# Kernel optimization log

Hardware: AMD Instinct MI355X
Metric: run time of the kernel (lower is better)

Reference implementation:

```python
import jax, jax.numpy as jnp
import numpy as np

# dims
B, S, V, H, D, I, L, SL, P = 1, 2048, 32000, 1024, 512, 4096, 2, 32, 4096
DECAY_FAST, DECAY_SLOW, CONS_RATE, CONS_EVERY = 0.9, 0.99, 0.1, 10


def _ln(x, g, b):
    m = x.mean(-1, keepdims=True)
    v = ((x - m) ** 2).mean(-1, keepdims=True)
    return (x - m) * jax.lax.rsqrt(v + 1e-5) * g + b


def _memory_scan(items, gates, fast0, slow0):
    # items [B,S,D], gates [B,S,SL]; sequential per-timestep memory update
    cons = (jnp.arange(items.shape[1]) % CONS_EVERY) == 0
    def step(carry, x):
        fast, slow = carry
        item, gate, c = x
        fast = DECAY_FAST * fast + gate[:, :, None] * item[:, None, :]
        slow = jnp.where(c, DECAY_SLOW * slow + CONS_RATE * fast, slow)
        fast = jnp.where(c, (1.0 - CONS_RATE) * fast, fast)
        return (fast, slow), None
    (fast, slow), _ = jax.lax.scan(
        step, (fast0, slow0),
        (items.transpose(1, 0, 2), gates.transpose(1, 0, 2), cons))
    return fast, slow


def _forward(input_ids, fast_states, slow_states, emb, pos_emb, W_item, b_item,
             W_q, b_q, rh_W1, rh_b1, rh_W2, rh_b2, gate_W, gate_b, W_out, b_out,
             ln1_g, ln1_b, ffn_W1, ffn_b1, ffn_W2, ffn_b2, ln2_g, ln2_b, fln_g, fln_b):
    b, s = input_ids.shape
    h = emb[input_ids] + pos_emb[:s][None]  # [B,S,H]
    new_fast, new_slow = [], []
    for l in range(W_item.shape[0]):
        items = h @ W_item[l] + b_item[l]          # [B,S,D]
        query = h @ W_q[l] + b_q[l]                # [B,S,H]
        # retrieval head -> unit-norm unbinding keys
        k1 = jax.nn.gelu(items @ rh_W1[l] + rh_b1[l])
        keys = k1 @ rh_W2[l] + rh_b2[l]
        keys = keys / (jnp.linalg.norm(keys, axis=-1, keepdims=True) + 1e-6)
        fast0, slow0 = fast_states[l], slow_states[l]  # [B,SL,D]
        # retrieval uses the initial (constant-within-sequence) states, so it
        # vectorizes over seq: slot attention + hadamard unbinding
        mem = jnp.concatenate([fast0, slow0], axis=1)  # [B,2*SL,D]
        scores = jnp.einsum('bsd,bnd->bsn', keys, mem) / jnp.sqrt(jnp.float32(D))
        attn = jax.nn.softmax(scores, axis=-1)
        retrieved = jnp.einsum('bsn,bnd->bsd', attn, mem) * keys  # [B,S,D]
        gates = jax.nn.sigmoid(jnp.concatenate([h, retrieved], -1) @ gate_W[l] + gate_b[l])
        fast_gates = gates[..., :SL]
        fast, slow = _memory_scan(items, fast_gates, fast0, slow0)
        new_fast.append(fast)
        new_slow.append(slow)
        out = jnp.concatenate([query, retrieved], -1) @ W_out[l] + b_out[l]
        h = _ln(h + out, ln1_g[l], ln1_b[l])
        ffn = jax.nn.gelu(h @ ffn_W1[l] + ffn_b1[l]) @ ffn_W2[l] + ffn_b2[l]
        h = _ln(h + ffn, ln2_g[l], ln2_b[l])
    h = _ln(h, fln_g, fln_b)
    logits = jnp.einsum('bsh,vh->bsv', h, emb)  # tied lm_head
    return logits, jnp.stack(new_fast), jnp.stack(new_slow)


def setup_inputs() -> dict:
    key = jax.random.key(0)
    def rn(i, shape, scale=0.02):
        return jax.random.normal(jax.random.fold_in(key, i), shape, dtype=jnp.float32) * scale
    z = lambda shape: jnp.zeros(shape, jnp.float32)
    return dict(
        input_ids=jax.random.randint(jax.random.fold_in(key, 0), (B, S), 0, V),
        fast_states=rn(100, (L, B, SL, D), 0.5),
        slow_states=rn(101, (L, B, SL, D), 0.5),
        emb=rn(1, (V, H)),
        pos_emb=rn(2, (P, H)),
        W_item=rn(3, (L, H, D)), b_item=z((L, D)),
        W_q=rn(4, (L, H, H)), b_q=z((L, H)),
        rh_W1=rn(5, (L, D, 2 * D)), rh_b1=z((L, 2 * D)),
        rh_W2=rn(6, (L, 2 * D, D)), rh_b2=z((L, D)),
        gate_W=rn(7, (L, H + D, 2 * SL)), gate_b=z((L, 2 * SL)),
        W_out=rn(8, (L, H + D, H)), b_out=z((L, H)),
        ln1_g=jnp.ones((L, H)), ln1_b=z((L, H)),
        ffn_W1=rn(9, (L, H, I)), ffn_b1=z((L, I)),
        ffn_W2=rn(10, (L, I, H)), ffn_b2=z((L, H)),
        ln2_g=jnp.ones((L, H)), ln2_b=z((L, H)),
        fln_g=jnp.ones((H,)), fln_b=z((H,)),
    )


def reference(input_ids, fast_states, slow_states, emb, pos_emb, W_item, b_item,
              W_q, b_q, rh_W1, rh_b1, rh_W2, rh_b2, gate_W, gate_b, W_out, b_out,
              ln1_g, ln1_b, ffn_W1, ffn_b1, ffn_W2, ffn_b2, ln2_g, ln2_b, fln_g, fln_b):
    return _forward(input_ids, fast_states, slow_states, emb, pos_emb, W_item, b_item,
                    W_q, b_q, rh_W1, rh_b1, rh_W2, rh_b2, gate_W, gate_b, W_out, b_out,
                    ln1_g, ln1_b, ffn_W1, ffn_b1, ffn_W2, ffn_b2, ln2_g, ln2_b, fln_g, fln_b)
```

## Files before the change

kernel.cpp:

```cpp
#include <hip/hip_runtime.h>
#include <hip/hip_bf16.h>
#include <stdint.h>

typedef __hip_bfloat16 bf16;
typedef float f32x4 __attribute__((ext_vector_type(4)));
typedef short s16x8 __attribute__((ext_vector_type(8)));
typedef short s16x4 __attribute__((ext_vector_type(4)));

#define DEV __device__ __forceinline__

static constexpr int S_ = 2048, H_ = 1024, D_ = 512, I_ = 4096, V_ = 32000;
static constexpr int SLn = 32, Lc = 2;
static constexpr size_t LOGITS_N = (size_t)S_ * V_;

DEV float gelu_f(float x) {
    float x3 = x * x * x;
    return 0.5f * x * (1.f + tanhf(0.7978845608028654f * (x + 0.044715f * x3)));
}

#define AS1(p) ((const __attribute__((address_space(1))) void*)(uintptr_t)(p))
#define AS3(p) ((__attribute__((address_space(3))) void*)(uint32_t)(uintptr_t)(p))

__global__ __launch_bounds__(512, 1) void logits_gemm(const bf16* __restrict__ A,
                                                      const bf16* __restrict__ BT,
                                                      float* __restrict__ C) {
    constexpr int NT = 32;
    __shared__ short lds[4 * 16384];
    const int tid = threadIdx.x, lane = tid & 63;
    const int wid = tid >> 6;
    const int wm = wid >> 2, wn = wid & 3;

    int bid = blockIdx.x;
    int wgid = (bid & 7) * 125 + (bid >> 3);
    const int m0 = (wgid & 7) * 256;
    const int n0 = (wgid >> 3) * 256;

    const int L = tid * 16;
    const int sidx = L >> 10, w = L & 1023;
    const int r16 = w >> 6;
    const int c2 = (w & 63) ^ (((r16 >> 3) & 1) << 5);
    const int srow = sidx * 16 + r16;
    const int scol = c2 >> 1;
    const bf16* aSrc[2];
    const bf16* bSrc[2];
#pragma unroll
    for (int h = 0; h < 2; ++h) {
        aSrc[h] = A + (size_t)(m0 + h * 128 + srow) * 1536 + scol;
        bSrc[h] = BT + (size_t)(n0 + h * 128 + srow) * 1024 + scol;
    }
    auto stage = [&](int kt) {
#pragma unroll
        for (int h = 0; h < 2; ++h) {
            __builtin_amdgcn_global_load_lds(AS1(aSrc[h] + kt * 32),
                                             AS3(&lds[(kt & 3) * 16384 + h * 4096 + tid * 8]), 16, 0, 0);
            __builtin_amdgcn_global_load_lds(AS1(bSrc[h] + kt * 32),
                                             AS3(&lds[(kt & 3) * 16384 + 8192 + h * 4096 + tid * 8]), 16, 0, 0);
        }
    };

    const int laneoff = (lane & 15) * 32 + (((lane >> 4) * 8) ^ (((lane >> 3) & 1) << 4));

    f32x4 acc[8][4];
#pragma unroll
    for (int i = 0; i < 8; i++)
#pragma unroll
        for (int j = 0; j < 4; j++)
#pragma unroll
            for (int r = 0; r < 4; r++) acc[i][j][r] = 0.f;

    s16x8 aE[8], bE[4], aO[8], bO[4];
    auto readE = [&](int kt) {
        const short* pa = &lds[(kt & 3) * 16384 + wm * 4096];
#pragma unroll
        for (int f = 0; f < 8; ++f) aE[f] = *(const s16x8*)&pa[(f >> 2) * 2048 + (f & 3) * 512 + laneoff];
        const short* pb = &lds[(kt & 3) * 16384 + 8192 + wn * 2048];
#pragma unroll
        for (int j = 0; j < 4; ++j) bE[j] = *(const s16x8*)&pb[j * 512 + laneoff];
    };
    auto readO = [&](int kt) {
        const short* pa = &lds[(kt & 3) * 16384 + wm * 4096];
#pragma unroll
        for (int f = 0; f < 8; ++f) aO[f] = *(const s16x8*)&pa[(f >> 2) * 2048 + (f & 3) * 512 + laneoff];
        const short* pb = &lds[(kt & 3) * 16384 + 8192 + wn * 2048];
#pragma unroll
        for (int j = 0; j < 4; ++j) bO[j] = *(const s16x8*)&pb[j * 512 + laneoff];
    };
    auto MM2E = [&]() {
        __builtin_amdgcn_s_setprio(1);
#pragma unroll
        for (int f = 0; f < 8; ++f)
#pragma unroll
            for (int j = 0; j < 4; ++j)
                acc[f][j] = __builtin_amdgcn_mfma_f32_16x16x32_bf16(aE[f], bE[j], acc[f][j], 0, 0, 0);
        __builtin_amdgcn_s_setprio(0);
    };
    auto MM2O = [&]() {
        __builtin_amdgcn_s_setprio(1);
#pragma unroll
        for (int f = 0; f < 8; ++f)
#pragma unroll
            for (int j = 0; j < 4; ++j)
                acc[f][j] = __builtin_amdgcn_mfma_f32_16x16x32_bf16(aO[f], bO[j], acc[f][j], 0, 0, 0);
        __builtin_amdgcn_s_setprio(0);
    };

#define GATE(tight)                                                     \
    do {                                                                \
        if (tight) asm volatile("s_waitcnt vmcnt(0)" ::: "memory");     \
        else       asm volatile("s_waitcnt vmcnt(4)" ::: "memory");     \
        __builtin_amdgcn_s_barrier();                                   \
        asm volatile("s_waitcnt lgkmcnt(0)" ::: "memory");              \
        __builtin_amdgcn_sched_barrier(0);                              \
    } while (0)
#define SB() __builtin_amdgcn_sched_barrier(0)

    stage(0);
    stage(1);
    stage(2);
    asm volatile("s_waitcnt vmcnt(8)" ::: "memory");
    __builtin_amdgcn_s_barrier();
    readE(0);

    for (int t = 0; t < NT; t += 2) {
        GATE(t >= NT - 2);
        readO(t + 1);
        SB();
        MM2E();
        if (t + 3 < NT) stage(t + 3);
        GATE(t + 1 >= NT - 2);
        if (t + 2 < NT) readE(t + 2);
        SB();
        MM2O();
        if (t + 4 < NT) stage(t + 4);
    }
#undef GATE
#undef SB

#pragma unroll
    for (int i = 0; i < 8; i++) {
        int gr0 = m0 + wm * 128 + i * 16 + ((lane >> 4) << 2);
#pragma unroll
        for (int j = 0; j < 4; j++) {
            int gc = n0 + wn * 64 + j * 16 + (lane & 15);
#pragma unroll
            for (int r = 0; r < 4; r++) C[(size_t)(gr0 + r) * V_ + gc] = acc[i][j][r];
        }
    }
}

template <int BM, int BN, int TH, int WM, int WN, int FLAGS>
__global__ __launch_bounds__(TH, 3) void gemm_p5(
    const bf16* __restrict__ A, int lda, const bf16* __restrict__ BT,
    const float* __restrict__ bias, const float* __restrict__ bias2,
    float* __restrict__ Cf, int ldf, bf16* __restrict__ Cb, int ldb2,
    bf16* __restrict__ Cb2, int K, int Mt, int Nt) {
    constexpr int FM = BM / (WM * 16), FN = BN / (WN * 16);
    constexpr int CA = (BM * 4) / TH, CB = (BN * 4) / TH, CH = CA + CB;
    constexpr int NPH = (FM * FN >= 32) ? 2 : 1;
    constexpr int FMP = FM / NPH;
    constexpr int BUFS = (BM + BN) * 32;
    __shared__ short lds[4 * BUFS];
    const int tid = threadIdx.x, lane = tid & 63;
    const int wm = (tid >> 6) / WN, wn = (tid >> 6) % WN;

    int nwg = Mt * Nt;
    int bid = blockIdx.x, wgid = bid;
    if ((nwg & 7) == 0) {
        int cpx = nwg >> 3;
        wgid = (bid & 7) * cpx + (bid >> 3);
    }
    const int m0 = (wgid % Mt) * BM, n0 = (wgid / Mt) * BN;

    const bf16* aS[CA];
    const bf16* bS[CB];
#pragma unroll
    for (int c = 0; c < CA; ++c) {
        int L = (c * TH + tid) * 16;
        int sidx = L >> 10, w = L & 1023;
        int r16 = w >> 6;
        int c2 = (w & 63) ^ (((r16 >> 3) & 1) << 5);
        aS[c] = A + (size_t)(m0 + sidx * 16 + r16) * lda + (c2 >> 1);
    }
#pragma unroll
    for (int c = 0; c < CB; ++c) {
        int L = (c * TH + tid) * 16;
        int sidx = L >> 10, w = L & 1023;
        int r16 = w >> 6;
        int c2 = (w & 63) ^ (((r16 >> 3) & 1) << 5);
        bS[c] = BT + (size_t)(n0 + sidx * 16 + r16) * K + (c2 >> 1);
    }

    auto stageA = [&](int kt) {
        short* dst = &lds[(kt & 3) * BUFS];
#pragma unroll
        for (int c = 0; c < CA; ++c)
            __builtin_amdgcn_global_load_lds(AS1(aS[c] + kt * 32), AS3(dst + (c * TH + tid) * 8), 16, 0, 0);
    };
    auto stageB = [&](int kt) {
        short* dst = &lds[(kt & 3) * BUFS + BM * 32];
#pragma unroll
        for (int c = 0; c < CB; ++c)
            __builtin_amdgcn_global_load_lds(AS1(bS[c] + kt * 32), AS3(dst + (c * TH + tid) * 8), 16, 0, 0);
    };

    const int laneoff = ((lane & 15) * 64 + ((((lane >> 4) * 8) ^ (((lane >> 3) & 1) << 4)) << 1)) >> 1;

    f32x4 acc[FM][FN];
#pragma unroll
    for (int i = 0; i < FM; i++)
#pragma unroll
        for (int j = 0; j < FN; j++)
#pragma unroll
            for (int r = 0; r < 4; r++) acc[i][j][r] = 0.f;

    const int NT = K >> 5;
    stageA(0); stageB(0);
    stageA(1); stageB(1);
    stageA(2); stageB(2);
    asm volatile("s_waitcnt vmcnt(%0)" ::"n"(2 * CH) : "memory");
    __builtin_amdgcn_s_barrier();
    for (int t = 0; t < NT; ++t) {
        const short* as = &lds[(t & 3) * BUFS];
        const short* bs = as + BM * 32;
        s16x8 bf[FN];
#pragma unroll
        for (int p = 0; p < NPH; ++p) {
            s16x8 af[FMP];
#pragma unroll
            for (int i = 0; i < FMP; i++)
                af[i] = *(const s16x8*)&as[(wm * FM + p * FMP + i) * 512 + laneoff];
            if (p == 0) {
#pragma unroll
                for (int j = 0; j < FN; j++)
                    bf[j] = *(const s16x8*)&bs[(wn * FN + j) * 512 + laneoff];
            }
            if (t + 3 < NT) {
                if (NPH == 1) {
                    stageA(t + 3);
                    stageB(t + 3);
                } else if (p == 0) {
                    stageA(t + 3);
                } else {
                    stageB(t + 3);
                }
            }
            if (p == NPH - 1) {
                const int rem = NT - 1 - t;
                if (rem >= 3)
                    asm volatile("s_waitcnt vmcnt(%0)" ::"n"(2 * CH) : "memory");
                else if (rem == 2)
                    asm volatile("s_waitcnt vmcnt(%0)" ::"n"(CH) : "memory");
                else
                    asm volatile("s_waitcnt vmcnt(0)" ::: "memory");
            }
            __builtin_amdgcn_s_barrier();
            __builtin_amdgcn_sched_barrier(0);
            __builtin_amdgcn_s_setprio(1);
#pragma unroll
            for (int i = 0; i < FMP; i++)
#pragma unroll
                for (int j = 0; j < FN; j++)
                    acc[p * FMP + i][j] =
                        __builtin_amdgcn_mfma_f32_16x16x32_bf16(af[i], bf[j], acc[p * FMP + i][j], 0, 0, 0);
            __builtin_amdgcn_s_setprio(0);
            __builtin_amdgcn_s_barrier();
        }
    }

#pragma unroll
    for (int i = 0; i < FM; i++) {
        int gr0 = m0 + (wm * FM + i) * 16 + ((lane >> 4) << 2);
#pragma unroll
        for (int j = 0; j < FN; j++) {
            int gc = n0 + (wn * FN + j) * 16 + (lane & 15);
            if (FLAGS & 32) {
                if (gc < 512) {
                    float bv = bias[gc];
#pragma unroll
                    for (int r = 0; r < 4; r++) {
                        float v = acc[i][j][r] + bv;
                        Cf[(size_t)(gr0 + r) * 512 + gc] = v;
                        Cb2[(size_t)(gr0 + r) * 512 + gc] = __float2bfloat16(v);
                    }
                } else {
                    float bv = bias2[gc - 512];
#pragma unroll
                    for (int r = 0; r < 4; r++)
                        Cb[(size_t)(gr0 + r) * 1536 + (gc - 512)] = __float2bfloat16(acc[i][j][r] + bv);
                }
            } else {
                float bv = (FLAGS & 1) ? bias[gc] : 0.f;
#pragma unroll
                for (int r = 0; r < 4; r++) {
                    float v = acc[i][j][r] + bv;
                    if (FLAGS & 2) v = gelu_f(v);
                    if (FLAGS & 4) Cf[(size_t)(gr0 + r) * ldf + gc] = v;
                    if (FLAGS & 8) Cb[(size_t)(gr0 + r) * ldb2 + gc] = __float2bfloat16(v);
                }
            }
        }
    }
}

__global__ __launch_bounds__(256) void transpose_bf16_kernel(const float* __restrict__ W,
                                                             bf16* __restrict__ WT, int K, int N) {
    __shared__ float t[32][33];
    int tx = threadIdx.x & 31, ty = threadIdx.x >> 5;
    int kb = blockIdx.y * 32, nb = blockIdx.x * 32;
#pragma unroll
    for (int i = 0; i < 4; i++)
        t[ty + 8 * i][tx] = W[(size_t)(kb + ty + 8 * i) * N + nb + tx];
    __syncthreads();
#pragma unroll
    for (int i = 0; i < 4; i++)
        WT[(size_t)(nb + ty + 8 * i) * K + kb + tx] = __float2bfloat16(t[tx][ty + 8 * i]);
}

__global__ void conv_bf16_kernel(const float* __restrict__ src, bf16* __restrict__ dst) {
    size_t i = (size_t)blockIdx.x * 256 + threadIdx.x;
    f32x4 v = ((const f32x4*)src)[i];
    s16x4 o;
#pragma unroll
    for (int j = 0; j < 4; j++) {
        bf16 h = __float2bfloat16(v[j]);
        o[j] = *(short*)&h;
    }
    ((s16x4*)dst)[i] = o;
}

__global__ void embed_kernel(const int* __restrict__ ids, const float* __restrict__ emb,
                             const float* __restrict__ pos, float* __restrict__ hF,
                             bf16* __restrict__ hB) {
    int t = blockIdx.x, tid = threadIdx.x;
    int id = ids[t];
    f32x4 v = ((const f32x4*)(emb + (size_t)id * H_))[tid];
    f32x4 q = ((const f32x4*)(pos + (size_t)t * H_))[tid];
    v = v + q;
    ((f32x4*)(hF + (size_t)t * H_))[tid] = v;
    s16x4 o;
#pragma unroll
    for (int j = 0; j < 4; j++) {
        bf16 h = __float2bfloat16(v[j]);
        o[j] = *(short*)&h;
    }
    ((s16x4*)(hB + (size_t)t * 1536))[tid] = o;
}

__global__ __launch_bounds__(256) void ln_kernel(const float* __restrict__ x,
                                                 const float* __restrict__ res,
                                                 const float* __restrict__ g,
                                                 const float* __restrict__ b,
                                                 float* __restrict__ of, bf16* __restrict__ ob,
                                                 int ldo) {
    __shared__ float red[8];
    int row = blockIdx.x, tid = threadIdx.x, lane = tid & 63, wid = tid >> 6;
    const float* xr = x + (size_t)row * H_;
    float v[4];
#pragma unroll
    for (int j = 0; j < 4; j++) {
        int c = tid + 256 * j;
        v[j] = xr[c] + (res ? res[(size_t)row * H_ + c] : 0.f);
    }
    float s = v[0] + v[1] + v[2] + v[3];
#pragma unroll
    for (int o = 32; o; o >>= 1) s += __shfl_xor(s, o);
    if (!lane) red[wid] = s;
    __syncthreads();
    float mean = (red[0] + red[1] + red[2] + red[3]) * (1.f / H_);
    float q = 0.f;
#pragma unroll
    for (int j = 0; j < 4; j++) {
        float d = v[j] - mean;
        q += d * d;
    }
#pragma unroll
    for (int o = 32; o; o >>= 1) q += __shfl_xor(q, o);
    if (!lane) red[4 + wid] = q;
    __syncthreads();
    float var = (red[4] + red[5] + red[6] + red[7]) * (1.f / H_);
    float rstd = rsqrtf(var + 1e-5f);
#pragma unroll
    for (int j = 0; j < 4; j++) {
        int c = tid + 256 * j;
        float o2 = (v[j] - mean) * rstd * g[c] + b[c];
        if (of) of[(size_t)row * H_ + c] = o2;
        if (ob) ob[(size_t)row * ldo + c] = __float2bfloat16(o2);
    }
}

__global__ void memt_kernel(const float* __restrict__ fast0, const float* __restrict__ slow0,
                            float* __restrict__ memT) {
    int idx = blockIdx.x * 256 + threadIdx.x;
    int d = idx >> 6, n = idx & 63;
    const float* m = (n < 32) ? fast0 + (size_t)n * D_ : slow0 + (size_t)(n - 32) * D_;
    memT[idx] = m[d];
}

__global__ __launch_bounds__(256) void attn_kernel(const float* __restrict__ keys,
                                                   const float* __restrict__ memT,
                                                   const float* __restrict__ fast0,
                                                   const float* __restrict__ slow0,
                                                   bf16* __restrict__ qr, bf16* __restrict__ hr) {
    __shared__ float klds[4][512];
    int wid = threadIdx.x >> 6, lane = threadIdx.x & 63;
    int r = blockIdx.x * 4 + wid;
    float kv[8], ss = 0.f;
#pragma unroll
    for (int j = 0; j < 8; j++) {
        kv[j] = keys[(size_t)r * D_ + lane + 64 * j];
        ss += kv[j] * kv[j];
    }
#pragma unroll
    for (int o = 32; o; o >>= 1) ss += __shfl_xor(ss, o);
    float inv = 1.f / (sqrtf(ss) + 1e-6f);
#pragma unroll
    for (int j = 0; j < 8; j++) {
        kv[j] *= inv;
        klds[wid][lane + 64 * j] = kv[j];
    }
    __syncthreads();
    float s0 = 0.f, s1 = 0.f, s2 = 0.f, s3 = 0.f;
#pragma unroll 8
    for (int d = 0; d < 512; d += 4) {
        s0 = fmaf(klds[wid][d + 0], memT[(d + 0) * 64 + lane], s0);
        s1 = fmaf(klds[wid][d + 1], memT[(d + 1) * 64 + lane], s1);
        s2 = fmaf(klds[wid][d + 2], memT[(d + 2) * 64 + lane], s2);
        s3 = fmaf(klds[wid][d + 3], memT[(d + 3) * 64 + lane], s3);
    }
    float s = (s0 + s1 + s2 + s3) * 0.044194173824159216f;
    float m = s;
#pragma unroll
    for (int o = 32; o; o >>= 1) m = fmaxf(m, __shfl_xor(m, o));
    float p = expf(s - m);
    float sum = p;
#pragma unroll
    for (int o = 32; o; o >>= 1) sum += __shfl_xor(sum, o);
    float pn = p / sum;
    float rv[8];
#pragma unroll
    for (int j = 0; j < 8; j++) rv[j] = 0.f;
    for (int n2 = 0; n2 < 64; ++n2) {
        float a2 = __shfl(pn, n2);
        const float* m2 = (n2 < 32) ? (fast0 + (size_t)n2 * D_) : (slow0 + (size_t)(n2 - 32) * D_);
#pragma unroll
        for (int j = 0; j < 8; j++) rv[j] = fmaf(a2, m2[lane + 64 * j], rv[j]);
    }
#pragma unroll
    for (int j = 0; j < 8; j++) {
        bf16 o = __float2bfloat16(rv[j] * kv[j]);
        qr[(size_t)r * 1536 + 1024 + lane + 64 * j] = o;
        hr[(size_t)r * 1536 + 1024 + lane + 64 * j] = o;
    }
}

__global__ void coef_kernel(float* __restrict__ coef) {
    int t = blockIdx.x * 256 + threadIdx.x;
    int j0 = (t + 9) / 10;
    float a = powf(0.9f, (float)(2047 - t + 205 - j0));
    float b = 0.f;
    for (int j = j0; j < 205; ++j)
        b += powf(0.9f, (float)(10 * j - t + j - j0)) * powf(0.99f, (float)(204 - j));
    b *= 0.1f;
    coef[t] = a;
    coef[2048 + t] = b;
    if (t == 0) {
        coef[4096] = powf(0.99f, 205.f);
        float cfs = 0.f;
        for (int j = 0; j < 205; ++j)
            cfs += powf(0.9f, (float)(11 * j + 1)) * powf(0.99f, (float)(204 - j));
        coef[4097] = 0.1f * cfs;
    }
}

__global__ void sigcoef_kernel(const float* __restrict__ raw, const float* __restrict__ coef,
                               float* __restrict__ ga, float* __restrict__ gb) {
    int i = blockIdx.x * 256 + threadIdx.x;
    int r = i >> 5, n = i & 31;
    float g = 1.f / (1.f + expf(-raw[r * 64 + n]));
    ga[i] = g * coef[r];
    gb[i] = g * coef[2048 + r];
}

__global__ __launch_bounds__(256) void scan_part_kernel(const float* __restrict__ items,
                                                        const float* __restrict__ ga,
                                                        const float* __restrict__ gb,
                                                        float* __restrict__ pF,
                                                        float* __restrict__ pS) {
    int tid = threadIdx.x;
    int d = (blockIdx.x & 7) * 64 + (tid & 63);
    int mg = (blockIdx.x >> 3) & 1;
    int tc = blockIdx.x >> 4;
    int m0 = mg * 16 + (tid >> 6) * 4;
    float aF[4] = {0.f, 0.f, 0.f, 0.f}, aS[4] = {0.f, 0.f, 0.f, 0.f};
    for (int t = tc * 128; t < tc * 128 + 128; ++t) {
        float it = items[(size_t)t * D_ + d];
#pragma unroll
        for (int j = 0; j < 4; j++) {
            aF[j] = fmaf(ga[t * 32 + m0 + j], it, aF[j]);
            aS[j] = fmaf(gb[t * 32 + m0 + j], it, aS[j]);
        }
    }
#pragma unroll
    for (int j = 0; j < 4; j++) {
        pF[((size_t)tc * 32 + m0 + j) * D_ + d] = aF[j];
        pS[((size_t)tc * 32 + m0 + j) * D_ + d] = aS[j];
    }
}

__global__ __launch_bounds__(256) void scan_reduce_kernel(const float* __restrict__ pF,
                                                          const float* __restrict__ pS,
                                                          const float* __restrict__ coef,
                                                          const float* __restrict__ fast0,
                                                          const float* __restrict__ slow0,
                                                          float* __restrict__ fastO,
                                                          float* __restrict__ slowO) {
    int i = blockIdx.x * 256 + threadIdx.x;
    float f = 0.f, s = 0.f;
#pragma unroll
    for (int c = 0; c < 16; c++) {
        f += pF[(size_t)c * 32 * D_ + i];
        s += pS[(size_t)c * 32 * D_ + i];
    }
    fastO[i] = f;
    slowO[i] = s + coef[4096] * slow0[i] + coef[4097] * fast0[i];
}

static inline void gemmM(hipStream_t st, const bf16* A, int lda, const bf16* BT,
                         const float* bias, const float* bias2, float* Cf, int ldf, bf16* Cb,
                         int ldb2, bf16* Cb2, int M, int N, int K, int flags) {
    if (N >= 1536 && (N % 128) == 0) {
        int Mt = M / 128, Nt = N / 128;
        dim3 g(Mt * Nt), b(256);
        if (flags == 33)
            gemm_p5<128, 128, 256, 2, 2, 33><<<g, b, 0, st>>>(A, lda, BT, bias, bias2, Cf, ldf,
                                                              Cb, ldb2, Cb2, K, Mt, Nt);
        else if (flags == 11)
            gemm_p5<128, 128, 256, 2, 2, 11><<<g, b, 0, st>>>(A, lda, BT, bias, bias2, Cf, ldf,
                                                              Cb, ldb2, Cb2, K, Mt, Nt);
        else
            gemm_p5<128, 128, 256, 2, 2, 5><<<g, b, 0, st>>>(A, lda, BT, bias, bias2, Cf, ldf,
                                                             Cb, ldb2, Cb2, K, Mt, Nt);
        return;
    }
    int Mt = M / 128, Nt = N / 64;
    dim3 g(Mt * Nt), b(256);
    if (flags == 11)
        gemm_p5<128, 64, 256, 2, 2, 11><<<g, b, 0, st>>>(A, lda, BT, bias, bias2, Cf, ldf, Cb,
                                                         ldb2, Cb2, K, Mt, Nt);
    else
        gemm_p5<128, 64, 256, 2, 2, 5><<<g, b, 0, st>>>(A, lda, BT, bias, bias2, Cf, ldf, Cb,
                                                        ldb2, Cb2, K, Mt, Nt);
}

static inline void transp(hipStream_t st, const float* W, bf16* WT, int K, int N) {
    transpose_bf16_kernel<<<dim3(N / 32, K / 32), 256, 0, st>>>(W, WT, K, N);
}

extern "C" void kernel_launch(void* const* d_in, const int* in_sizes, int n_in,
                              void* d_out, int out_size, void* d_ws, size_t ws_size,
                              hipStream_t stream) {
    const int* ids = (const int*)d_in[0];
    const float* fastS = (const float*)d_in[1];
    const float* slowS = (const float*)d_in[2];
    const float* emb = (const float*)d_in[3];
    const float* pos = (const float*)d_in[4];
    const float* W_item = (const float*)d_in[5];
    const float* b_item = (const float*)d_in[6];
    const float* W_q = (const float*)d_in[7];
    const float* b_q = (const float*)d_in[8];
    const float* rh_W1 = (const float*)d_in[9];
    const float* rh_b1 = (const float*)d_in[10];
    const float* rh_W2 = (const float*)d_in[11];
    const float* rh_b2 = (const float*)d_in[12];
    const float* gate_W = (const float*)d_in[13];
    const float* gate_b = (const float*)d_in[14];
    const float* W_out = (const float*)d_in[15];
    const float* b_out = (const float*)d_in[16];
    const float* ln1_g = (const float*)d_in[17];
    const float* ln1_b = (const float*)d_in[18];
    const float* ffn_W1 = (const float*)d_in[19];
    const float* ffn_b1 = (const float*)d_in[20];
    const float* ffn_W2 = (const float*)d_in[21];
    const float* ffn_b2 = (const float*)d_in[22];
    const float* ln2_g = (const float*)d_in[23];
    const float* ln2_b = (const float*)d_in[24];
    const float* fln_g = (const float*)d_in[25];
    const float* fln_b = (const float*)d_in[26];
    float* outP = (float*)d_out;

    size_t off = 0;
    char* base = (char*)d_ws;
    auto alloc = [&](size_t n) -> char* {
        char* p = base + off;
        off += (n + 255) & ~(size_t)255;
        return p;
    };
    bf16* wIQ = (bf16*)alloc((size_t)Lc * 1536 * H_ * 2);
    bf16* rh1T = (bf16*)alloc((size_t)Lc * (2 * D_) * D_ * 2);
    bf16* rh2T = (bf16*)alloc((size_t)Lc * D_ * (2 * D_) * 2);
    bf16* wOutT = (bf16*)alloc((size_t)Lc * H_ * 1536 * 2);
    bf16* f1T = (bf16*)alloc((size_t)Lc * I_ * H_ * 2);
    bf16* f2T = (bf16*)alloc((size_t)Lc * H_ * I_ * 2);
    bf16* gWT = (bf16*)alloc((size_t)Lc * 64 * 1536 * 2);
    bf16* embB = (bf16*)alloc((size_t)V_ * H_ * 2);
    float* hF = (float*)alloc((size_t)S_ * H_ * 4);
    bf16* hrB = (bf16*)alloc((size_t)S_ * 1536 * 2);
    bf16* hB = hrB;
    float* itemsF = (float*)alloc((size_t)S_ * D_ * 4);
    bf16* itemsB = (bf16*)alloc((size_t)S_ * D_ * 2);
    bf16* qrB = (bf16*)alloc((size_t)S_ * 1536 * 2);
    bf16* k1B = (bf16*)alloc((size_t)S_ * (2 * D_) * 2);
    float* keysF = (float*)alloc((size_t)S_ * D_ * 4);
    float* outF = (float*)alloc((size_t)S_ * H_ * 4);
    bf16* ffn1B = (bf16*)alloc((size_t)S_ * I_ * 2);
    float* gRawF = (float*)alloc((size_t)S_ * 64 * 4);
    float* gaF = (float*)alloc((size_t)S_ * SLn * 4);
    float* gbF = (float*)alloc((size_t)S_ * SLn * 4);
    float* coefF = (float*)alloc(4200 * 4);
    float* memT = (float*)alloc((size_t)D_ * 64 * 4);
    float* pF = (float*)alloc((size_t)16 * SLn * D_ * 4);
    float* pS = (float*)alloc((size_t)16 * SLn * D_ * 4);

    coef_kernel<<<8, 256, 0, stream>>>(coefF);
    for (int l = 0; l < Lc; ++l) {
        transp(stream, W_item + (size_t)l * H_ * D_, wIQ + (size_t)l * 1536 * H_, H_, D_);
        transp(stream, W_q + (size_t)l * H_ * H_, wIQ + (size_t)l * 1536 * H_ + (size_t)512 * H_,
               H_, H_);
        transp(stream, rh_W1 + (size_t)l * D_ * 2 * D_, rh1T + (size_t)l * 2 * D_ * D_, D_, 2 * D_);
        transp(stream, rh_W2 + (size_t)l * 2 * D_ * D_, rh2T + (size_t)l * D_ * 2 * D_, 2 * D_, D_);
        transp(stream, W_out + (size_t)l * 1536 * H_, wOutT + (size_t)l * H_ * 1536, 1536, H_);
        transp(stream, ffn_W1 + (size_t)l * H_ * I_, f1T + (size_t)l * I_ * H_, H_, I_);
        transp(stream, ffn_W2 + (size_t)l * I_ * H_, f2T + (size_t)l * H_ * I_, I_, H_);
        transp(stream, gate_W + (size_t)l * 1536 * 64, gWT + (size_t)l * 64 * 1536, 1536, 64);
    }
    conv_bf16_kernel<<<(int)((size_t)V_ * H_ / 4 / 256), 256, 0, stream>>>(emb, embB);
    embed_kernel<<<S_, 256, 0, stream>>>(ids, emb, pos, hF, hB);

    for (int l = 0; l < Lc; ++l) {
        const float* fast0 = fastS + (size_t)l * SLn * D_;
        const float* slow0 = slowS + (size_t)l * SLn * D_;
        gemmM(stream, hB, 1536, wIQ + (size_t)l * 1536 * H_, b_item + l * D_, b_q + l * H_,
              itemsF, 512, qrB, 1536, itemsB, S_, 1536, H_, 33);
        gemmM(stream, itemsB, D_, rh1T + (size_t)l * 2 * D_ * D_, rh_b1 + l * 2 * D_, nullptr,
              nullptr, 0, k1B, 2 * D_, nullptr, S_, 2 * D_, D_, 11);
        gemmM(stream, k1B, 2 * D_, rh2T + (size_t)l * D_ * 2 * D_, rh_b2 + l * D_, nullptr,
              keysF, D_, nullptr, 0, nullptr, S_, D_, 2 * D_, 5);
        memt_kernel<<<128, 256, 0, stream>>>(fast0, slow0, memT);
        attn_kernel<<<S_ / 4, 256, 0, stream>>>(keysF, memT, fast0, slow0, qrB, hrB);
        gemmM(stream, hrB, 1536, gWT + (size_t)l * 64 * 1536, gate_b + l * 64, nullptr, gRawF,
              64, nullptr, 0, nullptr, S_, 64, 1536, 5);
        sigcoef_kernel<<<S_ * SLn / 256, 256, 0, stream>>>(gRawF, coefF, gaF, gbF);
        scan_part_kernel<<<256, 256, 0, stream>>>(itemsF, gaF, gbF, pF, pS);
        scan_reduce_kernel<<<64, 256, 0, stream>>>(
            pF, pS, coefF, fast0, slow0, outP + LOGITS_N + (size_t)l * SLn * D_,
            outP + LOGITS_N + (size_t)Lc * SLn * D_ + (size_t)l * SLn * D_);
        gemmM(stream, qrB, 1536, wOutT + (size_t)l * H_ * 1536, b_out + l * H_, nullptr, outF,
              H_, nullptr, 0, nullptr, S_, H_, 1536, 5);
        ln_kernel<<<S_, 256, 0, stream>>>(hF, outF, ln1_g + l * H_, ln1_b + l * H_, hF, hB, 1536);
        gemmM(stream, hB, 1536, f1T + (size_t)l * I_ * H_, ffn_b1 + l * I_, nullptr, nullptr, 0,
              ffn1B, I_, nullptr, S_, I_, H_, 11);
        gemmM(stream, ffn1B, I_, f2T + (size_t)l * H_ * I_, ffn_b2 + l * H_, nullptr, outF, H_,
              nullptr, 0, nullptr, S_, H_, I_, 5);
        ln_kernel<<<S_, 256, 0, stream>>>(hF, outF, ln2_g + l * H_, ln2_b + l * H_, hF, hB, 1536);
    }
    ln_kernel<<<S_, 256, 0, stream>>>(hF, nullptr, fln_g, fln_b, nullptr, hB, 1536);
    logits_gemm<<<1000, 512, 0, stream>>>(hB, embB, outP);
}
```

Baseline: 901.7 us.

## Fuse gate projection with sigmoid, compute only used half, enlarge FFN1 tile

Replaces the 64-column gate GEMM plus the separate sigmoid/coefficient kernel with one warp-per-row kernel. It computes only the 32 gate columns the scan consumes, does the dot products in fp32 from bf16 inputs, and applies the sigmoid and decay coefficients in place. This removes a launch and the raw-logit buffer round trip, and halves the gate work. Separately, the N=4096 FFN1 GEMM now uses a 256x128 tile with min-waves 1, trading occupancy for more reuse per workgroup. The new kernel runs 32 serial shuffle reductions per row, and the larger tile may cut occupancy.

Result: slower. 1.108 ms (+22.8%).

```diff
diff --git a/kernel.cpp b/kernel.cpp
--- a/kernel.cpp
+++ b/kernel.cpp
@@ -148,8 +148,8 @@
     }
 }
 
-template <int BM, int BN, int TH, int WM, int WN, int FLAGS>
-__global__ __launch_bounds__(TH, 3) void gemm_p5(
+template <int BM, int BN, int TH, int WM, int WN, int MINW, int FLAGS>
+__global__ __launch_bounds__(TH, MINW) void gemm_p5(
     const bf16* __restrict__ A, int lda, const bf16* __restrict__ BT,
     const float* __restrict__ bias, const float* __restrict__ bias2,
     float* __restrict__ Cf, int ldf, bf16* __restrict__ Cb, int ldb2,
@@ -472,13 +472,59 @@
     }
 }
 
-__global__ void sigcoef_kernel(const float* __restrict__ raw, const float* __restrict__ coef,
-                               float* __restrict__ ga, float* __restrict__ gb) {
-    int i = blockIdx.x * 256 + threadIdx.x;
-    int r = i >> 5, n = i & 31;
-    float g = 1.f / (1.f + expf(-raw[r * 64 + n]));
-    ga[i] = g * coef[r];
-    gb[i] = g * coef[2048 + r];
+__global__ __launch_bounds__(256) void gates_kernel(const bf16* __restrict__ hrB,
+                                                    const bf16* __restrict__ gWT,
+                                                    const float* __restrict__ gBias,
+                                                    const float* __restrict__ coef,
+                                                    float* __restrict__ ga,
+                                                    float* __restrict__ gb) {
+    const int wid = threadIdx.x >> 6, lane = threadIdx.x & 63;
+    const int r = blockIdx.x * 4 + wid;
+    const bf16* hrow = hrB + (size_t)r * 1536 + lane * 24;
+    float hf[24];
+    {
+        s16x8 hv0 = *(const s16x8*)(hrow);
+        s16x8 hv1 = *(const s16x8*)(hrow + 8);
+        s16x8 hv2 = *(const s16x8*)(hrow + 16);
+#pragma unroll
+        for (int j = 0; j < 8; ++j) {
+            hf[j] = __uint_as_float((uint32_t)(uint16_t)hv0[j] << 16);
+            hf[8 + j] = __uint_as_float((uint32_t)(uint16_t)hv1[j] << 16);
+            hf[16 + j] = __uint_as_float((uint32_t)(uint16_t)hv2[j] << 16);
+        }
+    }
+    float acc[32];
+#pragma unroll
+    for (int n = 0; n < 32; ++n) acc[n] = 0.f;
+#pragma unroll
+    for (int n = 0; n < 32; ++n) {
+        const bf16* wrow = gWT + (size_t)n * 1536 + lane * 24;
+        s16x8 wv0 = *(const s16x8*)(wrow);
+        s16x8 wv1 = *(const s16x8*)(wrow + 8);
+        s16x8 wv2 = *(const s16x8*)(wrow + 16);
+        float a = acc[n];
+#pragma unroll
+        for (int j = 0; j < 8; ++j) {
+            a = fmaf(hf[j], __uint_as_float((uint32_t)(uint16_t)wv0[j] << 16), a);
+            a = fmaf(hf[8 + j], __uint_as_float((uint32_t)(uint16_t)wv1[j] << 16), a);
+            a = fmaf(hf[16 + j], __uint_as_float((uint32_t)(uint16_t)wv2[j] << 16), a);
+        }
+        acc[n] = a;
+    }
+#pragma unroll
+    for (int o = 32; o; o >>= 1) {
+#pragma unroll
+        for (int n = 0; n < 32; ++n) acc[n] += __shfl_xor(acc[n], o);
+    }
+    if (lane == 0) {
+        float ca = coef[r], cb = coef[2048 + r];
+#pragma unroll
+        for (int n = 0; n < 32; ++n) {
+            float g = 1.f / (1.f + expf(-(acc[n] + gBias[n])));
+            ga[r * 32 + n] = g * ca;
+            gb[r * 32 + n] = g * cb;
+        }
+    }
 }
 
 __global__ __launch_bounds__(256) void scan_part_kernel(const float* __restrict__ items,
@@ -528,28 +574,31 @@
 static inline void gemmM(hipStream_t st, const bf16* A, int lda, const bf16* BT,
                          const float* bias, const float* bias2, float* Cf, int ldf, bf16* Cb,
                          int ldb2, bf16* Cb2, int M, int N, int K, int flags) {
+    if (N == 4096) {
+        int Mt = M / 256, Nt = N / 128;
+        gemm_p5<256, 128, 256, 2, 2, 1, 11><<<dim3(Mt * Nt), 256, 0, st>>>(
+            A, lda, BT, bias, bias2, Cf, ldf, Cb, ldb2, Cb2, K, Mt, Nt);
+        return;
+    }
     if (N >= 1536 && (N % 128) == 0) {
         int Mt = M / 128, Nt = N / 128;
         dim3 g(Mt * Nt), b(256);
         if (flags == 33)
-            gemm_p5<128, 128, 256, 2, 2, 33><<<g, b, 0, st>>>(A, lda, BT, bias, bias2, Cf, ldf,
-                                                              Cb, ldb2, Cb2, K, Mt, Nt);
-        else if (flags == 11)
-            gemm_p5<128, 128, 256, 2, 2, 11><<<g, b, 0, st>>>(A, lda, BT, bias, bias2, Cf, ldf,
-                                                              Cb, ldb2, Cb2, K, Mt, Nt);
+            gemm_p5<128, 128, 256, 2, 2, 3, 33><<<g, b, 0, st>>>(A, lda, BT, bias, bias2, Cf,
+                                                                 ldf, Cb, ldb2, Cb2, K, Mt, Nt);
         else
-            gemm_p5<128, 128, 256, 2, 2, 5><<<g, b, 0, st>>>(A, lda, BT, bias, bias2, Cf, ldf,
-                                                             Cb, ldb2, Cb2, K, Mt, Nt);
+            gemm_p5<128, 128, 256, 2, 2, 3, 5><<<g, b, 0, st>>>(A, lda, BT, bias, bias2, Cf, ldf,
+                                                                Cb, ldb2, Cb2, K, Mt, Nt);
         return;
     }
     int Mt = M / 128, Nt = N / 64;
     dim3 g(Mt * Nt), b(256);
     if (flags == 11)
-        gemm_p5<128, 64, 256, 2, 2, 11><<<g, b, 0, st>>>(A, lda, BT, bias, bias2, Cf, ldf, Cb,
-                                                         ldb2, Cb2, K, Mt, Nt);
+        gemm_p5<128, 64, 256, 2, 2, 3, 11><<<g, b, 0, st>>>(A, lda, BT, bias, bias2, Cf, ldf, Cb,
+                                                            ldb2, Cb2, K, Mt, Nt);
     else
-        gemm_p5<128, 64, 256, 2, 2, 5><<<g, b, 0, st>>>(A, lda, BT, bias, bias2, Cf, ldf, Cb,
-                                                        ldb2, Cb2, K, Mt, Nt);
+        gemm_p5<128, 64, 256, 2, 2, 3, 5><<<g, b, 0, st>>>(A, lda, BT, bias, bias2, Cf, ldf, Cb,
+                                                           ldb2, Cb2, K, Mt, Nt);
 }
 
 static inline void transp(hipStream_t st, const float* W, bf16* WT, int K, int N) {
@@ -613,7 +662,6 @@
     float* keysF = (float*)alloc((size_t)S_ * D_ * 4);
     float* outF = (float*)alloc((size_t)S_ * H_ * 4);
     bf16* ffn1B = (bf16*)alloc((size_t)S_ * I_ * 2);
-    float* gRawF = (float*)alloc((size_t)S_ * 64 * 4);
     float* gaF = (float*)alloc((size_t)S_ * SLn * 4);
     float* gbF = (float*)alloc((size_t)S_ * SLn * 4);
     float* coefF = (float*)alloc(4200 * 4);
@@ -647,9 +695,8 @@
               keysF, D_, nullptr, 0, nullptr, S_, D_, 2 * D_, 5);
         memt_kernel<<<128, 256, 0, stream>>>(fast0, slow0, memT);
         attn_kernel<<<S_ / 4, 256, 0, stream>>>(keysF, memT, fast0, slow0, qrB, hrB);
-        gemmM(stream, hrB, 1536, gWT + (size_t)l * 64 * 1536, gate_b + l * 64, nullptr, gRawF,
-              64, nullptr, 0, nullptr, S_, 64, 1536, 5);
-        sigcoef_kernel<<<S_ * SLn / 256, 256, 0, stream>>>(gRawF, coefF, gaF, gbF);
+        gates_kernel<<<S_ / 4, 256, 0, stream>>>(hrB, gWT + (size_t)l * 64 * 1536,
+                                                 gate_b + l * 64, coefF, gaF, gbF);
         scan_part_kernel<<<256, 256, 0, stream>>>(itemsF, gaF, gbF, pF, pS);
         scan_reduce_kernel<<<64, 256, 0, stream>>>(
             pF, pS, coefF, fast0, slow0, outP + LOGITS_N + (size_t)l * SLn * D_,
```
